# Performance work log

Hardware: AMD Instinct MI355X
Metric: run time of the kernel (lower is better)

The kernel has to match this reference:

```python
import jax, jax.numpy as jnp
import numpy as np

B, SQ, SK, D, H = 4, 2048, 2048, 1024, 16
HD = D // H
LN_EPS = 1e-5


def setup_inputs() -> dict:
    key = jax.random.key(0)
    ks = jax.random.split(key, 16)
    s = 0.02
    return {
        "query": jax.random.normal(ks[0], (B, SQ, D), jnp.float32),
        "key": jax.random.normal(ks[1], (B, SK, D), jnp.float32),
        "value": jax.random.normal(ks[2], (B, SK, D), jnp.float32),
        "attention_mask": jax.random.randint(ks[3], (B, 1, 1, SK), 0, 2, jnp.int32),
        "relative_position_bias": jax.random.normal(ks[4], (1, H, SQ, SK), jnp.float32) * s,
        "Wq": jax.random.normal(ks[5], (D, D), jnp.float32) * s,
        "bq": jnp.zeros((D,), jnp.float32),
        "Wk": jax.random.normal(ks[6], (D, D), jnp.float32) * s,
        "bk": jnp.zeros((D,), jnp.float32),
        "Wv": jax.random.normal(ks[7], (D, D), jnp.float32) * s,
        "bv": jnp.zeros((D,), jnp.float32),
        "Wo": jax.random.normal(ks[8], (D, D), jnp.float32) * s,
        "bo": jnp.zeros((D,), jnp.float32),
        "ln_gamma": jnp.ones((D,), jnp.float32),
        "ln_beta": jnp.zeros((D,), jnp.float32),
    }


def reference(query, key, value, attention_mask, relative_position_bias,
              Wq, bq, Wk, bk, Wv, bv, Wo, bo, ln_gamma, ln_beta):
    # projections (torch Linear: x @ W.T + b)
    q = query @ Wq.T + bq   # [B,Sq,D]
    k = key @ Wk.T + bk     # [B,Sk,D]
    v = value @ Wv.T + bv   # [B,Sk,D]
    # split heads -> [B,H,S,hd]
    q = q.reshape(B, SQ, H, HD).transpose(0, 2, 1, 3)
    k = k.reshape(B, SK, H, HD).transpose(0, 2, 1, 3)
    v = v.reshape(B, SK, H, HD).transpose(0, 2, 1, 3)
    scores = jnp.einsum('bhqd,bhkd->bhqk', q, k) / jnp.sqrt(jnp.float32(HD))
    scores = scores + relative_position_bias
    scores = jnp.where(attention_mask == 0, -jnp.inf, scores)
    weights = jax.nn.softmax(scores, axis=-1)  # [B,H,Sq,Sk]
    ctx = jnp.einsum('bhqk,bhkd->bhqd', weights, v)
    ctx = ctx.transpose(0, 2, 1, 3).reshape(B, SQ, D)
    out = ctx @ Wo.T + bo
    x = query + out
    mu = jnp.mean(x, axis=-1, keepdims=True)
    var = jnp.var(x, axis=-1, keepdims=True)
    return (x - mu) * jax.lax.rsqrt(var + LN_EPS) * ln_gamma + ln_beta
```

## Files before the change

### kernel.cpp

```cpp
#include <hip/hip_runtime.h>
#include <hip/hip_bf16.h>

#define B_   4
#define SQ_  2048
#define SK_  2048
#define D_   1024
#define H_   16
#define HD_  64

#define LOG2E 1.4426950408889634f

typedef __bf16 bf16_t;
typedef bf16_t bf16x8 __attribute__((ext_vector_type(8)));
typedef bf16_t bf16x4 __attribute__((ext_vector_type(4)));
typedef float  f32x4  __attribute__((ext_vector_type(4)));
typedef int    i32x4  __attribute__((ext_vector_type(4)));
typedef unsigned u32x2 __attribute__((ext_vector_type(2)));



__device__ __forceinline__ void gll16(const bf16_t* g, bf16_t* l) {
    __builtin_amdgcn_global_load_lds(
        (const __attribute__((address_space(1))) unsigned int*)g,
        (__attribute__((address_space(3))) unsigned int*)l, 16, 0, 0);
}
__device__ __forceinline__ void gll16f(const float* g, float* l) {
    __builtin_amdgcn_global_load_lds(
        (const __attribute__((address_space(1))) unsigned int*)g,
        (__attribute__((address_space(3))) unsigned int*)l, 16, 0, 0);
}

__global__ __launch_bounds__(256) void cvt_bf16(
    const float* __restrict__ p0, const float* __restrict__ p1,
    const float* __restrict__ p2, const float* __restrict__ p3,
    bf16_t* __restrict__ d, int n)
{
    int y = blockIdx.y;
    const float* s = (y == 0) ? p0 : (y == 1) ? p1 : (y == 2) ? p2 : p3;
    int i = (blockIdx.x * 256 + threadIdx.x) * 8;
    f32x4 a = *(const f32x4*)(s + i);
    f32x4 b = *(const f32x4*)(s + i + 4);
    bf16x8 o;
    #pragma unroll
    for (int j = 0; j < 4; j++) { o[j] = (bf16_t)a[j]; o[4 + j] = (bf16_t)b[j]; }
    *(bf16x8*)(d + (size_t)y * n + i) = o;
}

__global__ __launch_bounds__(256) void gemm_qkv(
    const float* __restrict__ xq, const float* __restrict__ xk, const float* __restrict__ xv,
    const bf16_t* __restrict__ wb,
    const float* __restrict__ bq, const float* __restrict__ bk, const float* __restrict__ bv,
    bf16_t* __restrict__ oq, bf16_t* __restrict__ ok, bf16_t* __restrict__ ov)
{
    __shared__ __align__(16) float  lAf[2][4096];
    __shared__ __align__(16) bf16_t lB[2][4096];

    int z = blockIdx.z;
    const float* A = (z == 0) ? xq : (z == 1) ? xk : xv;
    const bf16_t* Bm = wb + (size_t)z * 1024 * 1024;
    const float* bias = (z == 0) ? bq : (z == 1) ? bk : bv;
    bf16_t* out = (z == 0) ? oq : (z == 1) ? ok : ov;

    int tid = threadIdx.x;
    int w = tid >> 6, l = tid & 63, lr = l & 15, lg = l >> 4;
    int m0 = blockIdx.x * 128, n0 = blockIdx.y * 128;
    int wm = (w >> 1) * 64, wn = (w & 1) * 64;

    f32x4 zero4 = {0.f, 0.f, 0.f, 0.f};
    f32x4 acc[4][4];
    #pragma unroll
    for (int i = 0; i < 4; i++)
        #pragma unroll
        for (int j = 0; j < 4; j++) acc[i][j] = zero4;

    int as0 = tid, as1 = tid + 256, as2 = tid + 512, as3 = tid + 768;
    int ar0 = as0 >> 3, ar1 = as1 >> 3, ar2 = as2 >> 3, ar3 = as3 >> 3;
    const float* a_p0 = A + (size_t)(m0 + ar0) * 1024 + (((as0 & 7) ^ (ar0 & 7)) * 4);
    const float* a_p1 = A + (size_t)(m0 + ar1) * 1024 + (((as1 & 7) ^ (ar1 & 7)) * 4);
    const float* a_p2 = A + (size_t)(m0 + ar2) * 1024 + (((as2 & 7) ^ (ar2 & 7)) * 4);
    const float* a_p3 = A + (size_t)(m0 + ar3) * 1024 + (((as3 & 7) ^ (ar3 & 7)) * 4);

    int bs0 = tid, bs1 = tid + 256;
    int br0 = bs0 >> 2, br1 = bs1 >> 2;
    const bf16_t* b_p0 = Bm + (size_t)(n0 + br0) * 1024 + (((bs0 & 3) ^ ((br0 >> 1) & 3)) * 8);
    const bf16_t* b_p1 = Bm + (size_t)(n0 + br1) * 1024 + (((bs1 & 3) ^ ((br1 >> 1) & 3)) * 8);

    auto stage = [&](int buf, int kt) {
        gll16f(a_p0 + kt * 32, &lAf[buf][as0 * 4]);
        gll16f(a_p1 + kt * 32, &lAf[buf][as1 * 4]);
        gll16f(a_p2 + kt * 32, &lAf[buf][as2 * 4]);
        gll16f(a_p3 + kt * 32, &lAf[buf][as3 * 4]);
        gll16(b_p0 + kt * 32, &lB[buf][bs0 * 8]);
        gll16(b_p1 + kt * 32, &lB[buf][bs1 * 8]);
    };

    stage(0, 0);
    int buf = 0;
    #pragma unroll 1
    for (int kt = 0; kt < 32; ++kt) {
        __syncthreads();
        if (kt + 1 < 32) stage(buf ^ 1, kt + 1);
        bf16x8 af[4], bfr[4];
        #pragma unroll
        for (int i = 0; i < 4; i++) {
            int ra = wm + i * 16 + lr;
            int e = ra & 7;
            const float* arow = &lAf[buf][ra * 32];
            f32x4 lo = *(const f32x4*)(arow + ((( lg * 2)      ^ e) * 4));
            f32x4 hi = *(const f32x4*)(arow + ((((lg * 2) + 1) ^ e) * 4));
            bf16x8 a8;
            #pragma unroll
            for (int j = 0; j < 4; j++) { a8[j] = (bf16_t)lo[j]; a8[4 + j] = (bf16_t)hi[j]; }
            af[i] = a8;
            int rb = wn + i * 16 + lr;
            bfr[i] = *(const bf16x8*)&lB[buf][rb * 32 + ((lg ^ ((rb >> 1) & 3)) * 8)];
        }
        #pragma unroll
        for (int mi = 0; mi < 4; mi++)
            #pragma unroll
            for (int ni = 0; ni < 4; ni++)
                acc[mi][ni] = __builtin_amdgcn_mfma_f32_16x16x32_bf16(af[mi], bfr[ni], acc[mi][ni], 0, 0, 0);
        buf ^= 1;
    }

    #pragma unroll
    for (int mi = 0; mi < 4; mi++) {
        int row = m0 + wm + mi * 16 + lg * 4;
        int bb_ = row >> 11;
        int s   = row & 2047;
        #pragma unroll
        for (int ni = 0; ni < 4; ni++) {
            int col = n0 + wn + ni * 16 + lr;
            int hh = col >> 6, d6 = col & 63;
            float bval = bias[col];
            if (z == 0) {
                size_t obase = (((size_t)bb_ * H_ + hh) * SQ_ + s) * HD_ + d6;
                #pragma unroll
                for (int r = 0; r < 4; r++)
                    out[obase + (size_t)r * HD_] =
                        (bf16_t)((acc[mi][ni][r] + bval) * (0.125f * LOG2E));
            } else if (z == 1) {
                int kt = s >> 6, kpb = s & 63;
                size_t tb = (((size_t)bb_ * H_ + hh) * 32 + kt) * 4096;
                #pragma unroll
                for (int r = 0; r < 4; r++) {
                    int kp = kpb + r;
                    out[tb + (size_t)kp * 64 + (((d6 >> 3) ^ (kp & 7)) * 8) + (d6 & 7)] =
                        (bf16_t)(acc[mi][ni][r] + bval);
                }
            } else {
                int kt = s >> 6, kpb = s & 63;
                int chunk = ((kpb >> 5) & 1) * 4 + ((kpb >> 2) & 3);
                int jb    = ((kpb >> 4) & 1) * 4;
                size_t tb = (((size_t)bb_ * H_ + hh) * 32 + kt) * 4096;
                bf16x4 o4;
                #pragma unroll
                for (int r = 0; r < 4; r++) o4[r] = (bf16_t)(acc[mi][ni][r] + bval);
                *(bf16x4*)(out + tb + (size_t)d6 * 64 + ((chunk ^ (d6 & 7)) * 8) + jb) = o4;
            }
        }
    }
}

__global__ __launch_bounds__(256) void gemm_out(
    const bf16_t* __restrict__ A, const bf16_t* __restrict__ Bm,
    const float* __restrict__ bias, const float* __restrict__ resid,
    bf16_t* __restrict__ out)
{
    __shared__ __align__(16) bf16_t lA[2][4096];
    __shared__ __align__(16) bf16_t lB[2][4096];

    int tid = threadIdx.x;
    int w = tid >> 6, l = tid & 63, lr = l & 15, lg = l >> 4;
    int m0 = blockIdx.x * 128, n0 = blockIdx.y * 128;
    int wm = (w >> 1) * 64, wn = (w & 1) * 64;

    f32x4 zero4 = {0.f, 0.f, 0.f, 0.f};
    f32x4 acc[4][4];
    #pragma unroll
    for (int i = 0; i < 4; i++)
        #pragma unroll
        for (int j = 0; j < 4; j++) acc[i][j] = zero4;

    int s0 = tid, s1 = 256 + tid;
    int r0 = s0 >> 2, c0 = s0 & 3, r1 = s1 >> 2, c1 = s1 & 3;
    const bf16_t* a0 = A + (size_t)(m0 + r0) * 1024 + ((c0 ^ ((r0 >> 1) & 3)) * 8);
    const bf16_t* a1 = A + (size_t)(m0 + r1) * 1024 + ((c1 ^ ((r1 >> 1) & 3)) * 8);
    const bf16_t* b0 = Bm + (size_t)(n0 + r0) * 1024 + ((c0 ^ ((r0 >> 1) & 3)) * 8);
    const bf16_t* b1 = Bm + (size_t)(n0 + r1) * 1024 + ((c1 ^ ((r1 >> 1) & 3)) * 8);

    auto stage = [&](int buf, int kt) {
        gll16(a0 + kt * 32, &lA[buf][s0 * 8]);
        gll16(a1 + kt * 32, &lA[buf][s1 * 8]);
        gll16(b0 + kt * 32, &lB[buf][s0 * 8]);
        gll16(b1 + kt * 32, &lB[buf][s1 * 8]);
    };

    stage(0, 0);
    int buf = 0;
    #pragma unroll 1
    for (int kt = 0; kt < 32; ++kt) {
        __syncthreads();
        if (kt + 1 < 32) stage(buf ^ 1, kt + 1);
        bf16x8 af[4], bfr[4];
        #pragma unroll
        for (int i = 0; i < 4; i++) {
            int ra = wm + i * 16 + lr;
            af[i] = *(const bf16x8*)&lA[buf][ra * 32 + ((lg ^ ((ra >> 1) & 3)) * 8)];
            int rb = wn + i * 16 + lr;
            bfr[i] = *(const bf16x8*)&lB[buf][rb * 32 + ((lg ^ ((rb >> 1) & 3)) * 8)];
        }
        #pragma unroll
        for (int mi = 0; mi < 4; mi++)
            #pragma unroll
            for (int ni = 0; ni < 4; ni++)
                acc[mi][ni] = __builtin_amdgcn_mfma_f32_16x16x32_bf16(af[mi], bfr[ni], acc[mi][ni], 0, 0, 0);
        buf ^= 1;
    }

    #pragma unroll
    for (int mi = 0; mi < 4; mi++) {
        int row = m0 + wm + mi * 16 + lg * 4;
        #pragma unroll
        for (int ni = 0; ni < 4; ni++) {
            int col = n0 + wn + ni * 16 + lr;
            float bval = bias[col];
            #pragma unroll
            for (int r = 0; r < 4; r++) {
                size_t o = (size_t)(row + r) * D_ + col;
                out[o] = (bf16_t)(acc[mi][ni][r] + bval + resid[o]);
            }
        }
    }
}

__global__ __launch_bounds__(512) void attn_kernel(
    const bf16_t* __restrict__ qg, const bf16_t* __restrict__ kgt,
    const bf16_t* __restrict__ vgt, const float* __restrict__ bias,
    const int* __restrict__ mask, bf16_t* __restrict__ ctx)
{
    __shared__ __align__(16) bf16_t ksh[2][8192];
    __shared__ __align__(16) bf16_t vsh[2][8192];
    __shared__ __align__(8) unsigned char mlds[256];

    int x = blockIdx.x;
    int g8 = x & 7;
    int rest = x >> 3;
    int b  = rest & 3;
    int tt = ((rest >> 2) << 3) | g8;
    int h  = tt >> 4;
    int qt = tt & 15;

    int tid = threadIdx.x;
    int w   = tid >> 6;
    int l   = tid & 63;
    int q16 = l & 15;
    int g   = l >> 4;
    int g4  = g * 4;

    int qrow = qt * 128 + w * 16 + q16;
    const bf16_t* qbase = qg + ((size_t)b * H_ + h) * SQ_ * HD_;
    bf16x8 qf0 = *(const bf16x8*)(qbase + (size_t)qrow * HD_ + g * 8);
    bf16x8 qf1 = *(const bf16x8*)(qbase + (size_t)qrow * HD_ + 32 + g * 8);

    const bf16_t* kt_base = kgt + ((size_t)b * H_ + h) * 32 * 4096;
    const bf16_t* vt_base = vgt + ((size_t)b * H_ + h) * 32 * 4096;
    const float* bias_row = bias + ((size_t)h * SQ_ + qrow) * SK_;

    f32x4 zero4 = {0.f, 0.f, 0.f, 0.f};
    f32x4 oacc[4];
    #pragma unroll
    for (int i = 0; i < 4; i++) oacc[i] = zero4;
    f32x4 lacc = zero4;

    bf16x8 ones;
    #pragma unroll
    for (int i = 0; i < 8; i++) ones[i] = (bf16_t)1.0f;

    auto stagePair = [&](int buf, int pt) {
        const bf16_t* ks = kt_base + (size_t)pt * 8192 + tid * 8;
        const bf16_t* vs = vt_base + (size_t)pt * 8192 + tid * 8;
        #pragma unroll
        for (int c = 0; c < 2; c++) {
            gll16(ks + c * 4096, &ksh[buf][c * 4096 + tid * 8]);
            gll16(vs + c * 4096, &vsh[buf][c * 4096 + tid * 8]);
        }
    };

    auto body = [&](const bf16_t* kb, const bf16_t* vb, int t) {
        f32x4 bb[4];
        const float* bp = bias_row + t * 64 + g4;
        #pragma unroll
        for (int ni = 0; ni < 4; ni++) bb[ni] = *(const f32x4*)(bp + ni * 16);
        u32x2 mm = *(const u32x2*)&mlds[t * 8];
        unsigned lo = mm[0], hi = mm[1];

        f32x4 s0[4];
        __builtin_amdgcn_s_setprio(1);
        #pragma unroll
        for (int ni = 0; ni < 4; ni++) {
            int krow = ni * 16 + q16;
            const bf16_t* kr = kb + krow * 64;
            bf16x8 kf0 = *(const bf16x8*)(kr + ((g       ^ (krow & 7)) * 8));
            bf16x8 kf1 = *(const bf16x8*)(kr + (((4 + g) ^ (krow & 7)) * 8));
            s0[ni] = zero4;
            s0[ni] = __builtin_amdgcn_mfma_f32_16x16x32_bf16(kf0, qf0, s0[ni], 0, 0, 0);
            s0[ni] = __builtin_amdgcn_mfma_f32_16x16x32_bf16(kf1, qf1, s0[ni], 0, 0, 0);
        }
        __builtin_amdgcn_s_setprio(0);

        unsigned n0_ = (lo >> g4) & 0xF;
        unsigned n1_ = (lo >> (16 + g4)) & 0xF;
        unsigned n2_ = (hi >> g4) & 0xF;
        unsigned n3_ = (hi >> (16 + g4)) & 0xF;

        bf16x8 pA0, pA1;
        #pragma unroll
        for (int r = 0; r < 4; r++) {
            float b0 = ((n0_ >> r) & 1) ? bb[0][r] : -30000.f;
            float b1 = ((n1_ >> r) & 1) ? bb[1][r] : -30000.f;
            float b2 = ((n2_ >> r) & 1) ? bb[2][r] : -30000.f;
            float b3 = ((n3_ >> r) & 1) ? bb[3][r] : -30000.f;
            pA0[r]     = (bf16_t)__builtin_amdgcn_exp2f(fmaf(b0, LOG2E, s0[0][r]));
            pA0[4 + r] = (bf16_t)__builtin_amdgcn_exp2f(fmaf(b1, LOG2E, s0[1][r]));
            pA1[r]     = (bf16_t)__builtin_amdgcn_exp2f(fmaf(b2, LOG2E, s0[2][r]));
            pA1[4 + r] = (bf16_t)__builtin_amdgcn_exp2f(fmaf(b3, LOG2E, s0[3][r]));
        }

        __builtin_amdgcn_s_setprio(1);
        lacc = __builtin_amdgcn_mfma_f32_16x16x32_bf16(ones, pA0, lacc, 0, 0, 0);
        lacc = __builtin_amdgcn_mfma_f32_16x16x32_bf16(ones, pA1, lacc, 0, 0, 0);
        #pragma unroll
        for (int nd = 0; nd < 4; nd++) {
            int vrow = nd * 16 + q16;
            const bf16_t* vr = vb + vrow * 64;
            bf16x8 vf0 = *(const bf16x8*)(vr + ((g       ^ (vrow & 7)) * 8));
            bf16x8 vf1 = *(const bf16x8*)(vr + (((4 + g) ^ (vrow & 7)) * 8));
            oacc[nd] = __builtin_amdgcn_mfma_f32_16x16x32_bf16(vf0, pA0, oacc[nd], 0, 0, 0);
            oacc[nd] = __builtin_amdgcn_mfma_f32_16x16x32_bf16(vf1, pA1, oacc[nd], 0, 0, 0);
        }
        __builtin_amdgcn_s_setprio(0);
    };

    stagePair(0, 0);
    if (tid < 256) {
        const int* mp = mask + (size_t)b * SK_ + tid * 8;
        i32x4 u0 = *(const i32x4*)mp;
        i32x4 u1 = *(const i32x4*)(mp + 4);
        unsigned by = 0;
        #pragma unroll
        for (int j = 0; j < 4; j++) by |= (u0[j] != 0 ? 1u : 0u) << j;
        #pragma unroll
        for (int j = 0; j < 4; j++) by |= (u1[j] != 0 ? 1u : 0u) << (4 + j);
        mlds[tid] = (unsigned char)by;
    }
    __syncthreads();

    #pragma unroll 1
    for (int pt = 0; pt < 16; ++pt) {
        int buf = pt & 1;
        if (pt + 1 < 16) stagePair(buf ^ 1, pt + 1);
        body(&ksh[buf][0],    &vsh[buf][0],    2 * pt);
        body(&ksh[buf][4096], &vsh[buf][4096], 2 * pt + 1);
        __syncthreads();
    }

    float l_r = lacc[0];
    float inv = (l_r > 0.f) ? 1.0f / l_r : 0.f;

    bf16_t* cp = ctx + ((size_t)b * SQ_ + qrow) * D_ + (size_t)h * HD_;
    #pragma unroll
    for (int nd = 0; nd < 4; nd++) {
        bf16x4 o4;
        #pragma unroll
        for (int r = 0; r < 4; r++) o4[r] = (bf16_t)(oacc[nd][r] * inv);
        *(bf16x4*)(cp + nd * 16 + g4) = o4;
    }
}

__global__ __launch_bounds__(256) void ln_kernel(
    const bf16_t* __restrict__ x, const float* __restrict__ gamma,
    const float* __restrict__ beta, float* __restrict__ out)
{
    int row = blockIdx.x;
    int t = threadIdx.x;
    const bf16_t* src = x + (size_t)row * D_;
    bf16x4 v4 = *(const bf16x4*)(src + t * 4);
    f32x4 v;
    #pragma unroll
    for (int i = 0; i < 4; i++) v[i] = (float)v4[i];
    float s  = v[0] + v[1] + v[2] + v[3];
    float s2 = v[0] * v[0] + v[1] * v[1] + v[2] * v[2] + v[3] * v[3];
    #pragma unroll
    for (int off = 32; off > 0; off >>= 1) {
        s  += __shfl_down(s, off);
        s2 += __shfl_down(s2, off);
    }
    __shared__ float red[8];
    int w = t >> 6, l = t & 63;
    if (l == 0) { red[w] = s; red[4 + w] = s2; }
    __syncthreads();
    if (t == 0) {
        red[0] = red[0] + red[1] + red[2] + red[3];
        red[4] = red[4] + red[5] + red[6] + red[7];
    }
    __syncthreads();
    float mu  = red[0] * (1.0f / D_);
    float var = red[4] * (1.0f / D_) - mu * mu;
    float rstd = rsqrtf(var + 1e-5f);
    f32x4 g  = *(const f32x4*)(gamma + t * 4);
    f32x4 be = *(const f32x4*)(beta + t * 4);
    f32x4 o;
    #pragma unroll
    for (int i = 0; i < 4; i++) o[i] = (v[i] - mu) * rstd * g[i] + be[i];
    *(f32x4*)(out + (size_t)row * D_ + t * 4) = o;
}

extern "C" void kernel_launch(void* const* d_in, const int* in_sizes, int n_in,
                              void* d_out, int out_size, void* d_ws, size_t ws_size,
                              hipStream_t stream)
{
    const float* query = (const float*)d_in[0];
    const float* key   = (const float*)d_in[1];
    const float* value = (const float*)d_in[2];
    const int*   mask  = (const int*)d_in[3];
    const float* bias  = (const float*)d_in[4];
    const float* Wq    = (const float*)d_in[5];
    const float* bq    = (const float*)d_in[6];
    const float* Wk    = (const float*)d_in[7];
    const float* bk    = (const float*)d_in[8];
    const float* Wv    = (const float*)d_in[9];
    const float* bv    = (const float*)d_in[10];
    const float* Wo    = (const float*)d_in[11];
    const float* bo    = (const float*)d_in[12];
    const float* gamma = (const float*)d_in[13];
    const float* beta  = (const float*)d_in[14];
    float* out = (float*)d_out;

    char* ws = (char*)d_ws;
    const size_t MB = 1024 * 1024;
    bf16_t* ctx = (bf16_t*)(ws);
    bf16_t* tmp = (bf16_t*)(ws + 16 * MB);
    bf16_t* wb  = (bf16_t*)(ws + 48 * MB);
    bf16_t* qb  = (bf16_t*)(ws + 56 * MB);
    bf16_t* kgt = (bf16_t*)(ws + 72 * MB);
    bf16_t* vgt = (bf16_t*)(ws + 88 * MB);

    cvt_bf16<<<dim3(512, 4), 256, 0, stream>>>(Wq, Wk, Wv, Wo, wb, 1024 * 1024);
    gemm_qkv<<<dim3(64, 8, 3), 256, 0, stream>>>(query, key, value, wb,
                                                 bq, bk, bv, qb, kgt, vgt);
    attn_kernel<<<dim3(1024), 512, 0, stream>>>(qb, kgt, vgt, bias, mask, ctx);
    gemm_out<<<dim3(64, 8), 256, 0, stream>>>(ctx, wb + (size_t)3 * 1024 * 1024, bo, query, tmp);
    ln_kernel<<<dim3(8192), 256, 0, stream>>>(tmp, gamma, beta, out);
}
```

Measured before the change: 303.8 us.

## Compact unmasked keys and run attention only over valid key tiles

Adds a mask_scan kernel that prefix-sums the attention mask per batch into compacted index and inverse-index tables plus a valid-key count. The QKV GEMM scatters K and V rows into compacted slots, and the attention loop iterates only over ceil(nkv/128) tile pairs, gathering bias values through the index table. This removes exp and MFMA work and K/V traffic for masked keys. In exchange, the bias becomes per-element gathered scalar loads and the V store loses its vector width. Padding slots in the last tile may hold stale K/V data, and only the -30000 bias keeps their softmax weight near zero.

```diff
diff --git a/kernel.cpp b/kernel.cpp
--- a/kernel.cpp
+++ b/kernel.cpp
@@ -15,7 +15,6 @@
 typedef bf16_t bf16x4 __attribute__((ext_vector_type(4)));
 typedef float  f32x4  __attribute__((ext_vector_type(4)));
 typedef int    i32x4  __attribute__((ext_vector_type(4)));
-typedef unsigned u32x2 __attribute__((ext_vector_type(2)));
 
 
 
@@ -28,6 +27,39 @@
     __builtin_amdgcn_global_load_lds(
         (const __attribute__((address_space(1))) unsigned int*)g,
         (__attribute__((address_space(3))) unsigned int*)l, 16, 0, 0);
+}
+
+__global__ __launch_bounds__(256) void mask_scan(
+    const int* __restrict__ mask, int* __restrict__ idx,
+    int* __restrict__ inv, int* __restrict__ nkv)
+{
+    int b = blockIdx.x;
+    const int* m = mask + (size_t)b * SK_;
+    int t = threadIdx.x;
+    __shared__ int cnt[257];
+    int bits[8];
+    int loc = 0;
+    #pragma unroll
+    for (int j = 0; j < 8; j++) { bits[j] = (m[t * 8 + j] != 0) ? 1 : 0; loc += bits[j]; }
+    cnt[t + 1] = loc;
+    __syncthreads();
+    if (t == 0) {
+        cnt[0] = 0;
+        for (int i = 1; i <= 256; i++) cnt[i] += cnt[i - 1];
+    }
+    __syncthreads();
+    int pos = cnt[t];
+    int* idxb = idx + (size_t)b * SK_;
+    int* invb = inv + (size_t)b * SK_;
+    #pragma unroll
+    for (int j = 0; j < 8; j++) {
+        int o = t * 8 + j;
+        if (bits[j]) { idxb[pos] = o; invb[o] = pos; pos++; }
+        else         { invb[o] = -1; }
+    }
+    int total = cnt[256];
+    if (t == 0) nkv[b] = total;
+    for (int s = total + t; s < SK_; s += 256) idxb[s] = 0;
 }
 
 __global__ __launch_bounds__(256) void cvt_bf16(
@@ -50,6 +82,7 @@
     const float* __restrict__ xq, const float* __restrict__ xk, const float* __restrict__ xv,
     const bf16_t* __restrict__ wb,
     const float* __restrict__ bq, const float* __restrict__ bk, const float* __restrict__ bv,
+    const int* __restrict__ inv,
     bf16_t* __restrict__ oq, bf16_t* __restrict__ ok, bf16_t* __restrict__ ov)
 {
     __shared__ __align__(16) float  lAf[2][4096];
@@ -128,6 +161,8 @@
         int row = m0 + wm + mi * 16 + lg * 4;
         int bb_ = row >> 11;
         int s   = row & 2047;
+        i32x4 sl4 = {0, 0, 0, 0};
+        if (z != 0) sl4 = *(const i32x4*)(inv + (size_t)bb_ * SK_ + s);
         #pragma unroll
         for (int ni = 0; ni < 4; ni++) {
             int col = n0 + wn + ni * 16 + lr;
@@ -140,23 +175,29 @@
                     out[obase + (size_t)r * HD_] =
                         (bf16_t)((acc[mi][ni][r] + bval) * (0.125f * LOG2E));
             } else if (z == 1) {
-                int kt = s >> 6, kpb = s & 63;
-                size_t tb = (((size_t)bb_ * H_ + hh) * 32 + kt) * 4096;
                 #pragma unroll
                 for (int r = 0; r < 4; r++) {
-                    int kp = kpb + r;
-                    out[tb + (size_t)kp * 64 + (((d6 >> 3) ^ (kp & 7)) * 8) + (d6 & 7)] =
-                        (bf16_t)(acc[mi][ni][r] + bval);
+                    int slot = sl4[r];
+                    if (slot >= 0) {
+                        int kt = slot >> 6, kpb = slot & 63;
+                        size_t tb = (((size_t)bb_ * H_ + hh) * 32 + kt) * 4096;
+                        out[tb + (size_t)kpb * 64 + (((d6 >> 3) ^ (kpb & 7)) * 8) + (d6 & 7)] =
+                            (bf16_t)(acc[mi][ni][r] + bval);
+                    }
                 }
             } else {
-                int kt = s >> 6, kpb = s & 63;
-                int chunk = ((kpb >> 5) & 1) * 4 + ((kpb >> 2) & 3);
-                int jb    = ((kpb >> 4) & 1) * 4;
-                size_t tb = (((size_t)bb_ * H_ + hh) * 32 + kt) * 4096;
-                bf16x4 o4;
                 #pragma unroll
-                for (int r = 0; r < 4; r++) o4[r] = (bf16_t)(acc[mi][ni][r] + bval);
-                *(bf16x4*)(out + tb + (size_t)d6 * 64 + ((chunk ^ (d6 & 7)) * 8) + jb) = o4;
+                for (int r = 0; r < 4; r++) {
+                    int slot = sl4[r];
+                    if (slot >= 0) {
+                        int kt = slot >> 6, v6 = slot & 63;
+                        int chunk = ((v6 >> 5) & 1) * 4 + ((v6 >> 2) & 3);
+                        int jj    = ((v6 >> 4) & 1) * 4 + (v6 & 3);
+                        size_t tb = (((size_t)bb_ * H_ + hh) * 32 + kt) * 4096;
+                        out[tb + (size_t)d6 * 64 + ((chunk ^ (d6 & 7)) * 8) + jj] =
+                            (bf16_t)(acc[mi][ni][r] + bval);
+                    }
+                }
             }
         }
     }
@@ -237,11 +278,12 @@
 __global__ __launch_bounds__(512) void attn_kernel(
     const bf16_t* __restrict__ qg, const bf16_t* __restrict__ kgt,
     const bf16_t* __restrict__ vgt, const float* __restrict__ bias,
-    const int* __restrict__ mask, bf16_t* __restrict__ ctx)
+    const int* __restrict__ idx, const int* __restrict__ nkvbuf,
+    bf16_t* __restrict__ ctx)
 {
     __shared__ __align__(16) bf16_t ksh[2][8192];
     __shared__ __align__(16) bf16_t vsh[2][8192];
-    __shared__ __align__(8) unsigned char mlds[256];
+    __shared__ __align__(16) int ilds[2048];
 
     int x = blockIdx.x;
     int g8 = x & 7;
@@ -258,6 +300,9 @@
     int g   = l >> 4;
     int g4  = g * 4;
 
+    int nkv = nkvbuf[b];
+    int nt  = (nkv + 127) >> 7;
+
     int qrow = qt * 128 + w * 16 + q16;
     const bf16_t* qbase = qg + ((size_t)b * H_ + h) * SQ_ * HD_;
     bf16x8 qf0 = *(const bf16x8*)(qbase + (size_t)qrow * HD_ + g * 8);
@@ -288,12 +333,18 @@
     };
 
     auto body = [&](const bf16_t* kb, const bf16_t* vb, int t) {
-        f32x4 bb[4];
-        const float* bp = bias_row + t * 64 + g4;
-        #pragma unroll
-        for (int ni = 0; ni < 4; ni++) bb[ni] = *(const f32x4*)(bp + ni * 16);
-        u32x2 mm = *(const u32x2*)&mlds[t * 8];
-        unsigned lo = mm[0], hi = mm[1];
+        int sb = t * 64;
+        float bv[4][4];
+        #pragma unroll
+        for (int ni = 0; ni < 4; ni++) {
+            #pragma unroll
+            for (int r = 0; r < 4; r++) {
+                int slot = sb + ni * 16 + g4 + r;
+                int col = ilds[slot];
+                float v = bias_row[col];
+                bv[ni][r] = (slot < nkv) ? v : -30000.f;
+            }
+        }
 
         f32x4 s0[4];
         __builtin_amdgcn_s_setprio(1);
@@ -309,22 +360,13 @@
         }
         __builtin_amdgcn_s_setprio(0);
 
-        unsigned n0_ = (lo >> g4) & 0xF;
-        unsigned n1_ = (lo >> (16 + g4)) & 0xF;
-        unsigned n2_ = (hi >> g4) & 0xF;
-        unsigned n3_ = (hi >> (16 + g4)) & 0xF;
-
         bf16x8 pA0, pA1;
         #pragma unroll
         for (int r = 0; r < 4; r++) {
-            float b0 = ((n0_ >> r) & 1) ? bb[0][r] : -30000.f;
-            float b1 = ((n1_ >> r) & 1) ? bb[1][r] : -30000.f;
-            float b2 = ((n2_ >> r) & 1) ? bb[2][r] : -30000.f;
-            float b3 = ((n3_ >> r) & 1) ? bb[3][r] : -30000.f;
-            pA0[r]     = (bf16_t)__builtin_amdgcn_exp2f(fmaf(b0, LOG2E, s0[0][r]));
-            pA0[4 + r] = (bf16_t)__builtin_amdgcn_exp2f(fmaf(b1, LOG2E, s0[1][r]));
-            pA1[r]     = (bf16_t)__builtin_amdgcn_exp2f(fmaf(b2, LOG2E, s0[2][r]));
-            pA1[4 + r] = (bf16_t)__builtin_amdgcn_exp2f(fmaf(b3, LOG2E, s0[3][r]));
+            pA0[r]     = (bf16_t)__builtin_amdgcn_exp2f(fmaf(bv[0][r], LOG2E, s0[0][r]));
+            pA0[4 + r] = (bf16_t)__builtin_amdgcn_exp2f(fmaf(bv[1][r], LOG2E, s0[1][r]));
+            pA1[r]     = (bf16_t)__builtin_amdgcn_exp2f(fmaf(bv[2][r], LOG2E, s0[2][r]));
+            pA1[4 + r] = (bf16_t)__builtin_amdgcn_exp2f(fmaf(bv[3][r], LOG2E, s0[3][r]));
         }
 
         __builtin_amdgcn_s_setprio(1);
@@ -343,23 +385,16 @@
     };
 
     stagePair(0, 0);
-    if (tid < 256) {
-        const int* mp = mask + (size_t)b * SK_ + tid * 8;
-        i32x4 u0 = *(const i32x4*)mp;
-        i32x4 u1 = *(const i32x4*)(mp + 4);
-        unsigned by = 0;
-        #pragma unroll
-        for (int j = 0; j < 4; j++) by |= (u0[j] != 0 ? 1u : 0u) << j;
-        #pragma unroll
-        for (int j = 0; j < 4; j++) by |= (u1[j] != 0 ? 1u : 0u) << (4 + j);
-        mlds[tid] = (unsigned char)by;
+    {
+        i32x4 v = *(const i32x4*)(idx + (size_t)b * SK_ + tid * 4);
+        *(i32x4*)&ilds[tid * 4] = v;
     }
     __syncthreads();
 
     #pragma unroll 1
-    for (int pt = 0; pt < 16; ++pt) {
+    for (int pt = 0; pt < nt; ++pt) {
         int buf = pt & 1;
-        if (pt + 1 < 16) stagePair(buf ^ 1, pt + 1);
+        if (pt + 1 < nt) stagePair(buf ^ 1, pt + 1);
         body(&ksh[buf][0],    &vsh[buf][0],    2 * pt);
         body(&ksh[buf][4096], &vsh[buf][4096], 2 * pt + 1);
         __syncthreads();
@@ -441,15 +476,19 @@
     const size_t MB = 1024 * 1024;
     bf16_t* ctx = (bf16_t*)(ws);
     bf16_t* tmp = (bf16_t*)(ws + 16 * MB);
+    int*    idx = (int*)(ws + 40 * MB);
+    int*    inv = (int*)(ws + 41 * MB);
+    int*    nkv = (int*)(ws + 42 * MB);
     bf16_t* wb  = (bf16_t*)(ws + 48 * MB);
     bf16_t* qb  = (bf16_t*)(ws + 56 * MB);
     bf16_t* kgt = (bf16_t*)(ws + 72 * MB);
     bf16_t* vgt = (bf16_t*)(ws + 88 * MB);
 
+    mask_scan<<<dim3(4), 256, 0, stream>>>(mask, idx, inv, nkv);
     cvt_bf16<<<dim3(512, 4), 256, 0, stream>>>(Wq, Wk, Wv, Wo, wb, 1024 * 1024);
     gemm_qkv<<<dim3(64, 8, 3), 256, 0, stream>>>(query, key, value, wb,
-                                                 bq, bk, bv, qb, kgt, vgt);
-    attn_kernel<<<dim3(1024), 512, 0, stream>>>(qb, kgt, vgt, bias, mask, ctx);
+                                                 bq, bk, bv, inv, qb, kgt, vgt);
+    attn_kernel<<<dim3(1024), 512, 0, stream>>>(qb, kgt, vgt, bias, idx, nkv, ctx);
     gemm_out<<<dim3(64, 8), 256, 0, stream>>>(ctx, wb + (size_t)3 * 1024 * 1024, bo, query, tmp);
     ln_kernel<<<dim3(8192), 256, 0, stream>>>(tmp, gamma, beta, out);
 }
```

New measurement: 441.1 us. 1.45x slower.
